# Kernel tuning notes

Hardware: AMD Instinct MI355X
Metric: run time of the kernel (lower is better)

Reference implementation:

```python
import jax, jax.numpy as jnp
import numpy as np

DELTA = 10.0
EPS = 1e-08
THRESHOLD = 0.9
STEEPNESS = 10.0


def setup_inputs() -> dict:
    key = jax.random.key(0)
    k1, k2 = jax.random.split(key)
    B, T2, T1, F = 16, 2048, 512, 128
    mels = jax.random.normal(k1, (B, T2, F), dtype=jnp.float32)
    alpha = jax.random.uniform(k2, (B, T2, T1), dtype=jnp.float32)
    mel_mask = jnp.ones((B, T2), dtype=jnp.int32)
    text_mask = jnp.ones((B, T1), dtype=jnp.int32)
    return {"mels": mels, "alpha": alpha, "mel_mask": mel_mask, "text_mask": text_mask}


def reference(mels, alpha, mel_mask, text_mask):
    B, T2, F = mels.shape
    T1 = text_mask.shape[-1]
    audio_mask = mel_mask.astype(bool)
    txt_mask = text_mask.astype(bool)
    am_f = audio_mask.astype(alpha.dtype)  # [B, T2]
    tm_f = txt_mask.astype(alpha.dtype)    # [B, T1]

    # index vector p: [B, T1]
    p = jnp.broadcast_to(jnp.arange(T1, dtype=alpha.dtype), (B, T1))

    # cosine similarity between consecutive frames (F.normalize: x / max(||x||, 1e-12))
    norm = jnp.maximum(jnp.linalg.norm(mels, axis=-1, keepdims=True), 1e-12)
    z_norm = mels / norm
    cosine_sim = jnp.sum(z_norm[:, :-1] * z_norm[:, 1:], axis=-1)  # [B, T2-1]
    activity = jax.nn.sigmoid(STEEPNESS * (THRESHOLD - cosine_sim))
    activity = jnp.concatenate([jnp.ones((B, 1), dtype=activity.dtype), activity], axis=-1)
    activity = activity * am_f

    # soft monotonic index via gated cumsum of alpha-proposal increments
    imv_proposal = jnp.einsum('bts,bs->bt', alpha, p)  # [B, T2]
    delta_prop = jnp.concatenate(
        [jnp.zeros((B, 1), dtype=imv_proposal.dtype), jnp.diff(imv_proposal, axis=-1)], axis=-1)
    eff_delta = jnp.clip(delta_prop * activity, 0.0, 1.0)
    imv = jnp.cumsum(eff_delta, axis=-1) * am_f

    # rescale so last valid frame maps to last phoneme index
    last_idx = jnp.maximum(audio_mask.sum(-1).astype(jnp.int32) - 1, 0)  # [B]
    last_val = jnp.maximum(jnp.take_along_axis(imv, last_idx[:, None], axis=1)[:, 0], 1e-06)
    text_len = txt_mask.sum(-1).astype(imv.dtype)
    scale = jnp.maximum(text_len - 1.0, 0.0) / last_val
    imv = imv * scale[:, None] * am_f

    # gamma: masked softmax over phonemes of -delta * (imv - p)^2
    dist_sq = (imv[:, :, None] - p[:, None, :]) ** 2  # [B, T2, T1]
    logits = jnp.where(txt_mask[:, None, :], -DELTA * dist_sq, -1e9)
    gamma = jax.nn.softmax(logits, axis=-1) * am_f[:, :, None]

    # durations: soft mass per phoneme
    durations = jnp.sum(gamma * am_f[:, :, None], axis=1) * tm_f  # [B, T1]

    # attention-pooling of mel frames onto phonemes
    w = jnp.swapaxes(gamma, 1, 2) * am_f[:, None, :]  # [B, T1, T2]
    w = w / (jnp.sum(w, axis=-1, keepdims=True) + EPS)
    aligned_mels = jnp.einsum('bst,btf->bsf', w, mels) * tm_f[:, :, None]  # [B, T1, F]
    return aligned_mels, durations, imv
```

## Files before the change

kernel.cpp:

```cpp
#include <hip/hip_runtime.h>
#include <math.h>
#include <cstddef>

#define B_  16
#define T2_ 2048
#define T1_ 512
#define F_  128

constexpr float DELTA_C  = 10.0f;
constexpr float EPS_C    = 1e-8f;
constexpr float THRESH_C = 0.9f;
constexpr float STEEP_C  = 10.0f;

typedef float f4v __attribute__((ext_vector_type(4)));

__global__ __launch_bounds__(256) void actprop_kernel(const float* __restrict__ mels,
                                                      const float* __restrict__ alpha,
                                                      const int* __restrict__ mel_mask,
                                                      float* __restrict__ act,
                                                      float* __restrict__ prop) {
    int wv   = (int)((blockIdx.x * blockDim.x + threadIdx.x) >> 6);
    int lane = threadIdx.x & 63;
    int il   = lane & 15;
    int r    = wv * 4 + (lane >> 4);
    int t    = r & (T2_ - 1);

    const f4v* arow = (const f4v*)(alpha + (size_t)r * T1_);
    f4v a0 = __builtin_nontemporal_load(&arow[il]);
    f4v a1 = __builtin_nontemporal_load(&arow[il + 16]);
    f4v a2 = __builtin_nontemporal_load(&arow[il + 32]);
    f4v a3 = __builtin_nontemporal_load(&arow[il + 48]);
    f4v a4 = __builtin_nontemporal_load(&arow[il + 64]);
    f4v a5 = __builtin_nontemporal_load(&arow[il + 80]);
    f4v a6 = __builtin_nontemporal_load(&arow[il + 96]);
    f4v a7 = __builtin_nontemporal_load(&arow[il + 112]);

    int rm = (t == 0) ? r : (r - 1);
    const f4v* my = (const f4v*)(mels + (size_t)r  * F_);
    const f4v* mx = (const f4v*)(mels + (size_t)rm * F_);
    f4v y0 = my[il * 2], y1 = my[il * 2 + 1];
    f4v x0 = mx[il * 2], x1 = mx[il * 2 + 1];

    float d  = x0.x*y0.x + x0.y*y0.y + x0.z*y0.z + x0.w*y0.w
             + x1.x*y1.x + x1.y*y1.y + x1.z*y1.z + x1.w*y1.w;
    float n0 = x0.x*x0.x + x0.y*x0.y + x0.z*x0.z + x0.w*x0.w
             + x1.x*x1.x + x1.y*x1.y + x1.z*x1.z + x1.w*x1.w;
    float n1 = y0.x*y0.x + y0.y*y0.y + y0.z*y0.z + y0.w*y0.w
             + y1.x*y1.x + y1.y*y1.y + y1.z*y1.z + y1.w*y1.w;

    float fb = (float)(il * 4);
    float psum;
    psum  = a0.x*(fb      ) + a0.y*(fb +   1.f) + a0.z*(fb +   2.f) + a0.w*(fb +   3.f);
    psum += a1.x*(fb+ 64.f) + a1.y*(fb +  65.f) + a1.z*(fb +  66.f) + a1.w*(fb +  67.f);
    psum += a2.x*(fb+128.f) + a2.y*(fb + 129.f) + a2.z*(fb + 130.f) + a2.w*(fb + 131.f);
    psum += a3.x*(fb+192.f) + a3.y*(fb + 193.f) + a3.z*(fb + 194.f) + a3.w*(fb + 195.f);
    psum += a4.x*(fb+256.f) + a4.y*(fb + 257.f) + a4.z*(fb + 258.f) + a4.w*(fb + 259.f);
    psum += a5.x*(fb+320.f) + a5.y*(fb + 321.f) + a5.z*(fb + 322.f) + a5.w*(fb + 323.f);
    psum += a6.x*(fb+384.f) + a6.y*(fb + 385.f) + a6.z*(fb + 386.f) + a6.w*(fb + 387.f);
    psum += a7.x*(fb+448.f) + a7.y*(fb + 449.f) + a7.z*(fb + 450.f) + a7.w*(fb + 451.f);

    for (int off = 8; off > 0; off >>= 1) {
        psum += __shfl_xor(psum, off, 64);
        d    += __shfl_xor(d,    off, 64);
        n0   += __shfl_xor(n0,   off, 64);
        n1   += __shfl_xor(n1,   off, 64);
    }

    if (il == 0) {
        float a_val;
        if (t == 0) {
            a_val = 1.0f;
        } else {
            float cs = d / (fmaxf(sqrtf(n0), 1e-12f) * fmaxf(sqrtf(n1), 1e-12f));
            a_val = 1.0f / (1.0f + __expf(-STEEP_C * (THRESH_C - cs)));
        }
        act[r]  = a_val * (float)mel_mask[r];
        prop[r] = psum;
    }
}

__global__ __launch_bounds__(512) void scan_kernel(const float* __restrict__ prop,
                                                   const float* __restrict__ act,
                                                   const int* __restrict__ mel_mask,
                                                   const int* __restrict__ text_mask,
                                                   float* __restrict__ imv_out,
                                                   float2* __restrict__ packed,
                                                   int2* __restrict__ bounds) {
    int b    = blockIdx.x;
    int tid  = threadIdx.x;
    int wave = tid >> 6, lane = tid & 63;
    __shared__ float s_imv[T2_];
    __shared__ float s_wsum[8];
    __shared__ int   s_am8[8], s_tm8[8];
    __shared__ int   s_tm[T1_];

    const float* pr = prop + (size_t)b * T2_;
    const float* ac = act  + (size_t)b * T2_;
    const int*   mm = mel_mask  + (size_t)b * T2_;
    const int*   tm = text_mask + (size_t)b * T1_;

    int tmv = tm[tid];
    s_tm[tid] = tmv;

    float e[4];
    int   mmv[4];
    int t0 = tid * 4;
    int am_local = 0;
    float run = 0.0f;
    for (int i = 0; i < 4; i++) {
        int t = t0 + i;
        float dd = (t == 0) ? 0.0f : (pr[t] - pr[t - 1]) * ac[t];
        dd = fminf(fmaxf(dd, 0.0f), 1.0f);
        run += dd;
        e[i] = run;
        mmv[i] = mm[t];
        am_local += mmv[i];
    }
    int tm_local = tmv;
    for (int off = 32; off > 0; off >>= 1) {
        am_local += __shfl_xor(am_local, off, 64);
        tm_local += __shfl_xor(tm_local, off, 64);
    }
    if (lane == 0) { s_am8[wave] = am_local; s_tm8[wave] = tm_local; }

    float v = run;
    for (int off = 1; off < 64; off <<= 1) {
        float u = __shfl_up(v, off, 64);
        if (lane >= off) v += u;
    }
    if (lane == 63) s_wsum[wave] = v;
    __syncthreads();

    float woff = 0.0f;
    for (int w = 0; w < 8; w++) woff += (w < wave) ? s_wsum[w] : 0.0f;
    float excl = woff + v - run;
    for (int i = 0; i < 4; i++) {
        int t = t0 + i;
        s_imv[t] = (e[i] + excl) * (float)mmv[i];
    }
    __syncthreads();

    int am_total = 0, tm_total = 0;
    for (int w = 0; w < 8; w++) { am_total += s_am8[w]; tm_total += s_tm8[w]; }
    int last_idx = max(am_total - 1, 0);
    float last_val = fmaxf(s_imv[last_idx], 1e-6f);
    float scale = fmaxf((float)tm_total - 1.0f, 0.0f) / last_val;
    __syncthreads();

    for (int i = 0; i < 4; i++) {
        int t = t0 + i;
        int valid = mmv[i];
        float vv = s_imv[t] * scale * (float)valid;
        imv_out[(size_t)b * T2_ + t] = vv;
        int c = (int)floorf(vv);
        float Z = 0.0f;
        for (int s = c - 2; s <= c + 3; s++) {
            if (s >= 0 && s < T1_ && s_tm[s]) {
                float dd = vv - (float)s;
                Z += __expf(-DELTA_C * dd * dd);
            }
        }
        Z = fmaxf(Z, 1e-30f);
        float key = valid ? vv : 3.0e4f;
        float2 pk = {key, valid ? (1.0f / Z) : 0.0f};
        packed[(size_t)b * T2_ + t] = pk;
        s_imv[t] = key;
    }
    __syncthreads();

    {
        int s = tid;
        float lov = (float)s - 3.0f, hiv = (float)s + 3.0f;
        int lo = 0, hi = T2_;
        while (lo < hi) { int mid = (lo + hi) >> 1; if (s_imv[mid] >= lov) hi = mid; else lo = mid + 1; }
        int st = lo;
        hi = T2_;
        while (lo < hi) { int mid = (lo + hi) >> 1; if (s_imv[mid] > hiv) hi = mid; else lo = mid + 1; }
        int2 be = {st, lo};
        bounds[(size_t)b * T1_ + s] = be;
    }
}

__global__ __launch_bounds__(256) void pool_kernel(const float* __restrict__ mels,
                                                   const int* __restrict__ text_mask,
                                                   const float2* __restrict__ packed,
                                                   const int2* __restrict__ bounds,
                                                   float* __restrict__ aligned,
                                                   float* __restrict__ dur) {
    int wid  = (int)((blockIdx.x * blockDim.x + threadIdx.x) >> 6);
    int lane = threadIdx.x & 63;
    if (wid >= B_ * (T1_ / 2)) return;
    int b = wid >> 8, s0 = (wid & 255) * 2;
    int half = lane >> 5, hl = lane & 31;
    float fs0 = (float)s0, fs1 = fs0 + 1.0f;

    const float2* pk   = packed + (size_t)b * T2_;
    const f4v*    mel4 = (const f4v*)(mels + (size_t)b * T2_ * F_);
    int2 b0 = bounds[(size_t)b * T1_ + s0];
    int2 b1 = bounds[(size_t)b * T1_ + s0 + 1];
    int t_lo = b0.x, t_hi = b1.y;

    float ax0 = 0.f, ay0 = 0.f, az0 = 0.f, aw0 = 0.f, g0s = 0.f;
    float ax1 = 0.f, ay1 = 0.f, az1 = 0.f, aw1 = 0.f, g1s = 0.f;
    for (int t = t_lo; t < t_hi; t += 2) {
        int  tl = t + half;
        bool on = tl < t_hi;
        int  ts = on ? tl : t;
        float2 p = pk[ts];
        f4v    m = mel4[(size_t)ts * 32 + hl];
        float d0 = p.x - fs0, d1 = p.x - fs1;
        float g0 = on ? __expf(-DELTA_C * d0 * d0) * p.y : 0.0f;
        float g1 = on ? __expf(-DELTA_C * d1 * d1) * p.y : 0.0f;
        g0s += g0; g1s += g1;
        ax0 += g0 * m.x; ay0 += g0 * m.y; az0 += g0 * m.z; aw0 += g0 * m.w;
        ax1 += g1 * m.x; ay1 += g1 * m.y; az1 += g1 * m.z; aw1 += g1 * m.w;
    }

    g0s += __shfl_xor(g0s, 32, 64);
    g1s += __shfl_xor(g1s, 32, 64);
    ax0 += __shfl_xor(ax0, 32, 64);
    ay0 += __shfl_xor(ay0, 32, 64);
    az0 += __shfl_xor(az0, 32, 64);
    aw0 += __shfl_xor(aw0, 32, 64);
    ax1 += __shfl_xor(ax1, 32, 64);
    ay1 += __shfl_xor(ay1, 32, 64);
    az1 += __shfl_xor(az1, 32, 64);
    aw1 += __shfl_xor(aw1, 32, 64);

    float tm0 = (float)text_mask[(size_t)b * T1_ + s0];
    float tm1 = (float)text_mask[(size_t)b * T1_ + s0 + 1];
    float inv0 = tm0 / (g0s + EPS_C);
    float inv1 = tm1 / (g1s + EPS_C);

    f4v out;
    if (half == 0) {
        out.x = ax0 * inv0; out.y = ay0 * inv0; out.z = az0 * inv0; out.w = aw0 * inv0;
    } else {
        out.x = ax1 * inv1; out.y = ay1 * inv1; out.z = az1 * inv1; out.w = aw1 * inv1;
    }
    float* obase = aligned + ((size_t)b * T1_ + s0 + half) * F_;
    ((f4v*)obase)[hl] = out;
    if (lane == 0)  dur[(size_t)b * T1_ + s0]     = g0s * tm0;
    if (lane == 32) dur[(size_t)b * T1_ + s0 + 1] = g1s * tm1;
}

extern "C" void kernel_launch(void* const* d_in, const int* in_sizes, int n_in,
                              void* d_out, int out_size, void* d_ws, size_t ws_size,
                              hipStream_t stream) {
    const float* mels      = (const float*)d_in[0];
    const float* alpha     = (const float*)d_in[1];
    const int*   mel_mask  = (const int*)d_in[2];
    const int*   text_mask = (const int*)d_in[3];

    float* out     = (float*)d_out;
    float* aligned = out;
    float* dur     = out + (size_t)B_ * T1_ * F_;
    float* imv     = dur + (size_t)B_ * T1_;

    float*  ws     = (float*)d_ws;
    float*  act    = ws;
    float*  prop   = ws + (size_t)B_ * T2_;
    float2* packed = (float2*)(ws + 2 * (size_t)B_ * T2_);
    int2*   bounds = (int2*)(ws + 4 * (size_t)B_ * T2_);

    actprop_kernel<<<(B_ * T2_) / 16, dim3(256), 0, stream>>>(mels, alpha, mel_mask, act, prop);
    scan_kernel   <<<B_,              dim3(512), 0, stream>>>(prop, act, mel_mask, text_mask, imv, packed, bounds);
    pool_kernel   <<<(B_ * T1_ / 2) / 4, dim3(256), 0, stream>>>(mels, text_mask, packed, bounds, aligned, dur);
}
```

Before: 128.4 us.

## Fuse activity, scan and pooling kernels into one flag-synchronized kernel

Merges the three kernels into one launch of 1024 blocks. Each block first computes activity and proposal values for 32 frames, then bumps a per-batch counter. One block per batch spins until all 64 blocks of that batch are done, runs the scan and bounds search with 256 threads (8 elements per thread), and releases a per-batch flag. The other blocks wait on that flag and then do the pooling. The aim is to drop the inter-kernel launch gaps and let batches proceed independently instead of stalling at global kernel boundaries. In exchange it needs every block resident at once to avoid deadlock, halves the scan's thread count, and adds a memset for the flags.

```diff
diff --git a/kernel.cpp b/kernel.cpp
--- a/kernel.cpp
+++ b/kernel.cpp
@@ -14,234 +14,258 @@
 
 typedef float f4v __attribute__((ext_vector_type(4)));
 
-__global__ __launch_bounds__(256) void actprop_kernel(const float* __restrict__ mels,
-                                                      const float* __restrict__ alpha,
-                                                      const int* __restrict__ mel_mask,
-                                                      float* __restrict__ act,
-                                                      float* __restrict__ prop) {
-    int wv   = (int)((blockIdx.x * blockDim.x + threadIdx.x) >> 6);
-    int lane = threadIdx.x & 63;
-    int il   = lane & 15;
-    int r    = wv * 4 + (lane >> 4);
-    int t    = r & (T2_ - 1);
-
-    const f4v* arow = (const f4v*)(alpha + (size_t)r * T1_);
-    f4v a0 = __builtin_nontemporal_load(&arow[il]);
-    f4v a1 = __builtin_nontemporal_load(&arow[il + 16]);
-    f4v a2 = __builtin_nontemporal_load(&arow[il + 32]);
-    f4v a3 = __builtin_nontemporal_load(&arow[il + 48]);
-    f4v a4 = __builtin_nontemporal_load(&arow[il + 64]);
-    f4v a5 = __builtin_nontemporal_load(&arow[il + 80]);
-    f4v a6 = __builtin_nontemporal_load(&arow[il + 96]);
-    f4v a7 = __builtin_nontemporal_load(&arow[il + 112]);
-
-    int rm = (t == 0) ? r : (r - 1);
-    const f4v* my = (const f4v*)(mels + (size_t)r  * F_);
-    const f4v* mx = (const f4v*)(mels + (size_t)rm * F_);
-    f4v y0 = my[il * 2], y1 = my[il * 2 + 1];
-    f4v x0 = mx[il * 2], x1 = mx[il * 2 + 1];
-
-    float d  = x0.x*y0.x + x0.y*y0.y + x0.z*y0.z + x0.w*y0.w
-             + x1.x*y1.x + x1.y*y1.y + x1.z*y1.z + x1.w*y1.w;
-    float n0 = x0.x*x0.x + x0.y*x0.y + x0.z*x0.z + x0.w*x0.w
-             + x1.x*x1.x + x1.y*x1.y + x1.z*x1.z + x1.w*x1.w;
-    float n1 = y0.x*y0.x + y0.y*y0.y + y0.z*y0.z + y0.w*y0.w
-             + y1.x*y1.x + y1.y*y1.y + y1.z*y1.z + y1.w*y1.w;
-
-    float fb = (float)(il * 4);
-    float psum;
-    psum  = a0.x*(fb      ) + a0.y*(fb +   1.f) + a0.z*(fb +   2.f) + a0.w*(fb +   3.f);
-    psum += a1.x*(fb+ 64.f) + a1.y*(fb +  65.f) + a1.z*(fb +  66.f) + a1.w*(fb +  67.f);
-    psum += a2.x*(fb+128.f) + a2.y*(fb + 129.f) + a2.z*(fb + 130.f) + a2.w*(fb + 131.f);
-    psum += a3.x*(fb+192.f) + a3.y*(fb + 193.f) + a3.z*(fb + 194.f) + a3.w*(fb + 195.f);
-    psum += a4.x*(fb+256.f) + a4.y*(fb + 257.f) + a4.z*(fb + 258.f) + a4.w*(fb + 259.f);
-    psum += a5.x*(fb+320.f) + a5.y*(fb + 321.f) + a5.z*(fb + 322.f) + a5.w*(fb + 323.f);
-    psum += a6.x*(fb+384.f) + a6.y*(fb + 385.f) + a6.z*(fb + 386.f) + a6.w*(fb + 387.f);
-    psum += a7.x*(fb+448.f) + a7.y*(fb + 449.f) + a7.z*(fb + 450.f) + a7.w*(fb + 451.f);
-
-    for (int off = 8; off > 0; off >>= 1) {
-        psum += __shfl_xor(psum, off, 64);
-        d    += __shfl_xor(d,    off, 64);
-        n0   += __shfl_xor(n0,   off, 64);
-        n1   += __shfl_xor(n1,   off, 64);
-    }
-
-    if (il == 0) {
-        float a_val;
-        if (t == 0) {
-            a_val = 1.0f;
-        } else {
-            float cs = d / (fmaxf(sqrtf(n0), 1e-12f) * fmaxf(sqrtf(n1), 1e-12f));
-            a_val = 1.0f / (1.0f + __expf(-STEEP_C * (THRESH_C - cs)));
-        }
-        act[r]  = a_val * (float)mel_mask[r];
-        prop[r] = psum;
-    }
-}
-
-__global__ __launch_bounds__(512) void scan_kernel(const float* __restrict__ prop,
-                                                   const float* __restrict__ act,
-                                                   const int* __restrict__ mel_mask,
-                                                   const int* __restrict__ text_mask,
-                                                   float* __restrict__ imv_out,
-                                                   float2* __restrict__ packed,
-                                                   int2* __restrict__ bounds) {
-    int b    = blockIdx.x;
-    int tid  = threadIdx.x;
-    int wave = tid >> 6, lane = tid & 63;
+__global__ __launch_bounds__(256, 4) void fused_kernel(
+        const float* __restrict__ mels,
+        const float* __restrict__ alpha,
+        const int* __restrict__ mel_mask,
+        const int* __restrict__ text_mask,
+        float* __restrict__ act,
+        float* __restrict__ prop,
+        float* __restrict__ imv_out,
+        float2* __restrict__ packed,
+        int2* __restrict__ bounds,
+        float* __restrict__ aligned,
+        float* __restrict__ dur,
+        int* done_act,
+        int* scan_done)
+{
     __shared__ float s_imv[T2_];
-    __shared__ float s_wsum[8];
-    __shared__ int   s_am8[8], s_tm8[8];
+    __shared__ float s_wsum[4];
+    __shared__ int   s_am4[4], s_tm4[4];
     __shared__ int   s_tm[T1_];
 
-    const float* pr = prop + (size_t)b * T2_;
-    const float* ac = act  + (size_t)b * T2_;
-    const int*   mm = mel_mask  + (size_t)b * T2_;
-    const int*   tm = text_mask + (size_t)b * T1_;
-
-    int tmv = tm[tid];
-    s_tm[tid] = tmv;
-
-    float e[4];
-    int   mmv[4];
-    int t0 = tid * 4;
-    int am_local = 0;
-    float run = 0.0f;
-    for (int i = 0; i < 4; i++) {
-        int t = t0 + i;
-        float dd = (t == 0) ? 0.0f : (pr[t] - pr[t - 1]) * ac[t];
-        dd = fminf(fmaxf(dd, 0.0f), 1.0f);
-        run += dd;
-        e[i] = run;
-        mmv[i] = mm[t];
-        am_local += mmv[i];
-    }
-    int tm_local = tmv;
-    for (int off = 32; off > 0; off >>= 1) {
-        am_local += __shfl_xor(am_local, off, 64);
-        tm_local += __shfl_xor(tm_local, off, 64);
-    }
-    if (lane == 0) { s_am8[wave] = am_local; s_tm8[wave] = tm_local; }
-
-    float v = run;
-    for (int off = 1; off < 64; off <<= 1) {
-        float u = __shfl_up(v, off, 64);
-        if (lane >= off) v += u;
-    }
-    if (lane == 63) s_wsum[wave] = v;
-    __syncthreads();
-
-    float woff = 0.0f;
-    for (int w = 0; w < 8; w++) woff += (w < wave) ? s_wsum[w] : 0.0f;
-    float excl = woff + v - run;
-    for (int i = 0; i < 4; i++) {
-        int t = t0 + i;
-        s_imv[t] = (e[i] + excl) * (float)mmv[i];
+    const int g    = blockIdx.x;
+    const int b    = g >> 6;
+    const int tid  = threadIdx.x;
+    const int wv   = tid >> 6, lane = tid & 63;
+    const int il   = lane & 15, sub = lane >> 4;
+
+    #pragma unroll
+    for (int p = 0; p < 2; ++p) {
+        int r = g * 32 + p * 16 + wv * 4 + sub;
+        int t = r & (T2_ - 1);
+
+        const f4v* arow = (const f4v*)(alpha + (size_t)r * T1_);
+        f4v a0 = __builtin_nontemporal_load(&arow[il]);
+        f4v a1 = __builtin_nontemporal_load(&arow[il + 16]);
+        f4v a2 = __builtin_nontemporal_load(&arow[il + 32]);
+        f4v a3 = __builtin_nontemporal_load(&arow[il + 48]);
+        f4v a4 = __builtin_nontemporal_load(&arow[il + 64]);
+        f4v a5 = __builtin_nontemporal_load(&arow[il + 80]);
+        f4v a6 = __builtin_nontemporal_load(&arow[il + 96]);
+        f4v a7 = __builtin_nontemporal_load(&arow[il + 112]);
+
+        int rm = (t == 0) ? r : (r - 1);
+        const f4v* my = (const f4v*)(mels + (size_t)r  * F_);
+        const f4v* mx = (const f4v*)(mels + (size_t)rm * F_);
+        f4v y0 = my[il * 2], y1 = my[il * 2 + 1];
+        f4v x0 = mx[il * 2], x1 = mx[il * 2 + 1];
+
+        float d  = x0.x*y0.x + x0.y*y0.y + x0.z*y0.z + x0.w*y0.w
+                 + x1.x*y1.x + x1.y*y1.y + x1.z*y1.z + x1.w*y1.w;
+        float n0 = x0.x*x0.x + x0.y*x0.y + x0.z*x0.z + x0.w*x0.w
+                 + x1.x*x1.x + x1.y*x1.y + x1.z*x1.z + x1.w*x1.w;
+        float n1 = y0.x*y0.x + y0.y*y0.y + y0.z*y0.z + y0.w*y0.w
+                 + y1.x*y1.x + y1.y*y1.y + y1.z*y1.z + y1.w*y1.w;
+
+        float fb = (float)(il * 4);
+        float psum;
+        psum  = a0.x*(fb      ) + a0.y*(fb +   1.f) + a0.z*(fb +   2.f) + a0.w*(fb +   3.f);
+        psum += a1.x*(fb+ 64.f) + a1.y*(fb +  65.f) + a1.z*(fb +  66.f) + a1.w*(fb +  67.f);
+        psum += a2.x*(fb+128.f) + a2.y*(fb + 129.f) + a2.z*(fb + 130.f) + a2.w*(fb + 131.f);
+        psum += a3.x*(fb+192.f) + a3.y*(fb + 193.f) + a3.z*(fb + 194.f) + a3.w*(fb + 195.f);
+        psum += a4.x*(fb+256.f) + a4.y*(fb + 257.f) + a4.z*(fb + 258.f) + a4.w*(fb + 259.f);
+        psum += a5.x*(fb+320.f) + a5.y*(fb + 321.f) + a5.z*(fb + 322.f) + a5.w*(fb + 323.f);
+        psum += a6.x*(fb+384.f) + a6.y*(fb + 385.f) + a6.z*(fb + 386.f) + a6.w*(fb + 387.f);
+        psum += a7.x*(fb+448.f) + a7.y*(fb + 449.f) + a7.z*(fb + 450.f) + a7.w*(fb + 451.f);
+
+        for (int off = 8; off > 0; off >>= 1) {
+            psum += __shfl_xor(psum, off, 64);
+            d    += __shfl_xor(d,    off, 64);
+            n0   += __shfl_xor(n0,   off, 64);
+            n1   += __shfl_xor(n1,   off, 64);
+        }
+
+        if (il == 0) {
+            float a_val;
+            if (t == 0) {
+                a_val = 1.0f;
+            } else {
+                float cs = d / (fmaxf(sqrtf(n0), 1e-12f) * fmaxf(sqrtf(n1), 1e-12f));
+                a_val = 1.0f / (1.0f + __expf(-STEEP_C * (THRESH_C - cs)));
+            }
+            act[r]  = a_val * (float)mel_mask[r];
+            prop[r] = psum;
+        }
     }
     __syncthreads();
-
-    int am_total = 0, tm_total = 0;
-    for (int w = 0; w < 8; w++) { am_total += s_am8[w]; tm_total += s_tm8[w]; }
-    int last_idx = max(am_total - 1, 0);
-    float last_val = fmaxf(s_imv[last_idx], 1e-6f);
-    float scale = fmaxf((float)tm_total - 1.0f, 0.0f) / last_val;
-    __syncthreads();
-
-    for (int i = 0; i < 4; i++) {
-        int t = t0 + i;
-        int valid = mmv[i];
-        float vv = s_imv[t] * scale * (float)valid;
-        imv_out[(size_t)b * T2_ + t] = vv;
-        int c = (int)floorf(vv);
-        float Z = 0.0f;
-        for (int s = c - 2; s <= c + 3; s++) {
-            if (s >= 0 && s < T1_ && s_tm[s]) {
-                float dd = vv - (float)s;
-                Z += __expf(-DELTA_C * dd * dd);
+    if (tid == 0)
+        __hip_atomic_fetch_add(&done_act[b], 1, __ATOMIC_RELEASE, __HIP_MEMORY_SCOPE_AGENT);
+
+    const bool is_scan = ((g & 63) == 0);
+
+    if (is_scan) {
+        const int* tm = text_mask + (size_t)b * T1_;
+        int tmv0 = tm[tid], tmv1 = tm[tid + 256];
+        s_tm[tid] = tmv0; s_tm[tid + 256] = tmv1;
+
+        if (lane == 0) {
+            while (__hip_atomic_load(&done_act[b], __ATOMIC_RELAXED, __HIP_MEMORY_SCOPE_AGENT) < 64)
+                __builtin_amdgcn_s_sleep(2);
+        }
+        __builtin_amdgcn_fence(__ATOMIC_ACQUIRE, "agent");
+        __syncthreads();
+
+        const float* pr_ = prop + (size_t)b * T2_;
+        const float* ac_ = act  + (size_t)b * T2_;
+        const int*   mm_ = mel_mask + (size_t)b * T2_;
+
+        float e[8];
+        int   mmv[8];
+        int t0 = tid * 8;
+        int am_local = 0;
+        float run = 0.0f;
+        #pragma unroll
+        for (int i = 0; i < 8; i++) {
+            int t = t0 + i;
+            float dd = (t == 0) ? 0.0f : (pr_[t] - pr_[t - 1]) * ac_[t];
+            dd = fminf(fmaxf(dd, 0.0f), 1.0f);
+            run += dd;
+            e[i] = run;
+            mmv[i] = mm_[t];
+            am_local += mmv[i];
+        }
+        int tm_local = tmv0 + tmv1;
+        for (int off = 32; off > 0; off >>= 1) {
+            am_local += __shfl_xor(am_local, off, 64);
+            tm_local += __shfl_xor(tm_local, off, 64);
+        }
+        if (lane == 0) { s_am4[wv] = am_local; s_tm4[wv] = tm_local; }
+
+        float v = run;
+        for (int off = 1; off < 64; off <<= 1) {
+            float u = __shfl_up(v, off, 64);
+            if (lane >= off) v += u;
+        }
+        if (lane == 63) s_wsum[wv] = v;
+        __syncthreads();
+
+        float woff = 0.0f;
+        for (int w = 0; w < 4; w++) woff += (w < wv) ? s_wsum[w] : 0.0f;
+        float excl = woff + v - run;
+        #pragma unroll
+        for (int i = 0; i < 8; i++) {
+            int t = t0 + i;
+            s_imv[t] = (e[i] + excl) * (float)mmv[i];
+        }
+        __syncthreads();
+
+        int am_total = s_am4[0] + s_am4[1] + s_am4[2] + s_am4[3];
+        int tm_total = s_tm4[0] + s_tm4[1] + s_tm4[2] + s_tm4[3];
+        int last_idx = max(am_total - 1, 0);
+        float last_val = fmaxf(s_imv[last_idx], 1e-6f);
+        float scale = fmaxf((float)tm_total - 1.0f, 0.0f) / last_val;
+        __syncthreads();
+
+        #pragma unroll
+        for (int i = 0; i < 8; i++) {
+            int t = t0 + i;
+            int valid = mmv[i];
+            float vv = s_imv[t] * scale * (float)valid;
+            imv_out[(size_t)b * T2_ + t] = vv;
+            int c = (int)floorf(vv);
+            float Z = 0.0f;
+            for (int s = c - 2; s <= c + 3; s++) {
+                if (s >= 0 && s < T1_ && s_tm[s]) {
+                    float dd = vv - (float)s;
+                    Z += __expf(-DELTA_C * dd * dd);
+                }
             }
-        }
-        Z = fmaxf(Z, 1e-30f);
-        float key = valid ? vv : 3.0e4f;
-        float2 pk = {key, valid ? (1.0f / Z) : 0.0f};
-        packed[(size_t)b * T2_ + t] = pk;
-        s_imv[t] = key;
+            Z = fmaxf(Z, 1e-30f);
+            float key = valid ? vv : 3.0e4f;
+            float2 pkv = {key, valid ? (1.0f / Z) : 0.0f};
+            packed[(size_t)b * T2_ + t] = pkv;
+            s_imv[t] = key;
+        }
+        __syncthreads();
+
+        for (int k = 0; k < 2; k++) {
+            int s = tid + k * 256;
+            float lov = (float)s - 3.0f, hiv = (float)s + 3.0f;
+            int lo = 0, hi = T2_;
+            while (lo < hi) { int mid = (lo + hi) >> 1; if (s_imv[mid] >= lov) hi = mid; else lo = mid + 1; }
+            int st = lo;
+            hi = T2_;
+            while (lo < hi) { int mid = (lo + hi) >> 1; if (s_imv[mid] > hiv) hi = mid; else lo = mid + 1; }
+            int2 be = {st, lo};
+            bounds[(size_t)b * T1_ + s] = be;
+        }
+        __syncthreads();
+        if (tid == 0)
+            __hip_atomic_store(&scan_done[b], 1, __ATOMIC_RELEASE, __HIP_MEMORY_SCOPE_AGENT);
+    } else {
+        if (lane == 0) {
+            while (__hip_atomic_load(&scan_done[b], __ATOMIC_RELAXED, __HIP_MEMORY_SCOPE_AGENT) == 0)
+                __builtin_amdgcn_s_sleep(2);
+        }
+        __builtin_amdgcn_fence(__ATOMIC_ACQUIRE, "agent");
     }
-    __syncthreads();
 
     {
-        int s = tid;
-        float lov = (float)s - 3.0f, hiv = (float)s + 3.0f;
-        int lo = 0, hi = T2_;
-        while (lo < hi) { int mid = (lo + hi) >> 1; if (s_imv[mid] >= lov) hi = mid; else lo = mid + 1; }
-        int st = lo;
-        hi = T2_;
-        while (lo < hi) { int mid = (lo + hi) >> 1; if (s_imv[mid] > hiv) hi = mid; else lo = mid + 1; }
-        int2 be = {st, lo};
-        bounds[(size_t)b * T1_ + s] = be;
+        int pairi = (g & 63) * 4 + wv;
+        int s0 = pairi * 2;
+        int half = lane >> 5, hl = lane & 31;
+        float fs0 = (float)s0, fs1 = fs0 + 1.0f;
+
+        const float2* pk   = packed + (size_t)b * T2_;
+        const f4v*    mel4 = (const f4v*)(mels + (size_t)b * T2_ * F_);
+        int2 b0 = bounds[(size_t)b * T1_ + s0];
+        int2 b1 = bounds[(size_t)b * T1_ + s0 + 1];
+        int t_lo = b0.x, t_hi = b1.y;
+
+        float ax0 = 0.f, ay0 = 0.f, az0 = 0.f, aw0 = 0.f, g0s = 0.f;
+        float ax1 = 0.f, ay1 = 0.f, az1 = 0.f, aw1 = 0.f, g1s = 0.f;
+        for (int t = t_lo; t < t_hi; t += 2) {
+            int  tl = t + half;
+            bool on = tl < t_hi;
+            int  ts = on ? tl : t;
+            float2 p = pk[ts];
+            f4v    m = mel4[(size_t)ts * 32 + hl];
+            float d0 = p.x - fs0, d1 = p.x - fs1;
+            float g0 = on ? __expf(-DELTA_C * d0 * d0) * p.y : 0.0f;
+            float g1 = on ? __expf(-DELTA_C * d1 * d1) * p.y : 0.0f;
+            g0s += g0; g1s += g1;
+            ax0 += g0 * m.x; ay0 += g0 * m.y; az0 += g0 * m.z; aw0 += g0 * m.w;
+            ax1 += g1 * m.x; ay1 += g1 * m.y; az1 += g1 * m.z; aw1 += g1 * m.w;
+        }
+
+        g0s += __shfl_xor(g0s, 32, 64);
+        g1s += __shfl_xor(g1s, 32, 64);
+        ax0 += __shfl_xor(ax0, 32, 64);
+        ay0 += __shfl_xor(ay0, 32, 64);
+        az0 += __shfl_xor(az0, 32, 64);
+        aw0 += __shfl_xor(aw0, 32, 64);
+        ax1 += __shfl_xor(ax1, 32, 64);
+        ay1 += __shfl_xor(ay1, 32, 64);
+        az1 += __shfl_xor(az1, 32, 64);
+        aw1 += __shfl_xor(aw1, 32, 64);
+
+        float tm0 = (float)text_mask[(size_t)b * T1_ + s0];
+        float tm1 = (float)text_mask[(size_t)b * T1_ + s0 + 1];
+        float inv0 = tm0 / (g0s + EPS_C);
+        float inv1 = tm1 / (g1s + EPS_C);
+
+        f4v outv;
+        if (half == 0) {
+            outv.x = ax0 * inv0; outv.y = ay0 * inv0; outv.z = az0 * inv0; outv.w = aw0 * inv0;
+        } else {
+            outv.x = ax1 * inv1; outv.y = ay1 * inv1; outv.z = az1 * inv1; outv.w = aw1 * inv1;
+        }
+        float* obase = aligned + ((size_t)b * T1_ + s0 + half) * F_;
+        ((f4v*)obase)[hl] = outv;
+        if (lane == 0)  dur[(size_t)b * T1_ + s0]     = g0s * tm0;
+        if (lane == 32) dur[(size_t)b * T1_ + s0 + 1] = g1s * tm1;
     }
-}
-
-__global__ __launch_bounds__(256) void pool_kernel(const float* __restrict__ mels,
-                                                   const int* __restrict__ text_mask,
-                                                   const float2* __restrict__ packed,
-                                                   const int2* __restrict__ bounds,
-                                                   float* __restrict__ aligned,
-                                                   float* __restrict__ dur) {
-    int wid  = (int)((blockIdx.x * blockDim.x + threadIdx.x) >> 6);
-    int lane = threadIdx.x & 63;
-    if (wid >= B_ * (T1_ / 2)) return;
-    int b = wid >> 8, s0 = (wid & 255) * 2;
-    int half = lane >> 5, hl = lane & 31;
-    float fs0 = (float)s0, fs1 = fs0 + 1.0f;
-
-    const float2* pk   = packed + (size_t)b * T2_;
-    const f4v*    mel4 = (const f4v*)(mels + (size_t)b * T2_ * F_);
-    int2 b0 = bounds[(size_t)b * T1_ + s0];
-    int2 b1 = bounds[(size_t)b * T1_ + s0 + 1];
-    int t_lo = b0.x, t_hi = b1.y;
-
-    float ax0 = 0.f, ay0 = 0.f, az0 = 0.f, aw0 = 0.f, g0s = 0.f;
-    float ax1 = 0.f, ay1 = 0.f, az1 = 0.f, aw1 = 0.f, g1s = 0.f;
-    for (int t = t_lo; t < t_hi; t += 2) {
-        int  tl = t + half;
-        bool on = tl < t_hi;
-        int  ts = on ? tl : t;
-        float2 p = pk[ts];
-        f4v    m = mel4[(size_t)ts * 32 + hl];
-        float d0 = p.x - fs0, d1 = p.x - fs1;
-        float g0 = on ? __expf(-DELTA_C * d0 * d0) * p.y : 0.0f;
-        float g1 = on ? __expf(-DELTA_C * d1 * d1) * p.y : 0.0f;
-        g0s += g0; g1s += g1;
-        ax0 += g0 * m.x; ay0 += g0 * m.y; az0 += g0 * m.z; aw0 += g0 * m.w;
-        ax1 += g1 * m.x; ay1 += g1 * m.y; az1 += g1 * m.z; aw1 += g1 * m.w;
-    }
-
-    g0s += __shfl_xor(g0s, 32, 64);
-    g1s += __shfl_xor(g1s, 32, 64);
-    ax0 += __shfl_xor(ax0, 32, 64);
-    ay0 += __shfl_xor(ay0, 32, 64);
-    az0 += __shfl_xor(az0, 32, 64);
-    aw0 += __shfl_xor(aw0, 32, 64);
-    ax1 += __shfl_xor(ax1, 32, 64);
-    ay1 += __shfl_xor(ay1, 32, 64);
-    az1 += __shfl_xor(az1, 32, 64);
-    aw1 += __shfl_xor(aw1, 32, 64);
-
-    float tm0 = (float)text_mask[(size_t)b * T1_ + s0];
-    float tm1 = (float)text_mask[(size_t)b * T1_ + s0 + 1];
-    float inv0 = tm0 / (g0s + EPS_C);
-    float inv1 = tm1 / (g1s + EPS_C);
-
-    f4v out;
-    if (half == 0) {
-        out.x = ax0 * inv0; out.y = ay0 * inv0; out.z = az0 * inv0; out.w = aw0 * inv0;
-    } else {
-        out.x = ax1 * inv1; out.y = ay1 * inv1; out.z = az1 * inv1; out.w = aw1 * inv1;
-    }
-    float* obase = aligned + ((size_t)b * T1_ + s0 + half) * F_;
-    ((f4v*)obase)[hl] = out;
-    if (lane == 0)  dur[(size_t)b * T1_ + s0]     = g0s * tm0;
-    if (lane == 32) dur[(size_t)b * T1_ + s0 + 1] = g1s * tm1;
 }
 
 extern "C" void kernel_launch(void* const* d_in, const int* in_sizes, int n_in,
@@ -262,8 +286,11 @@
     float*  prop   = ws + (size_t)B_ * T2_;
     float2* packed = (float2*)(ws + 2 * (size_t)B_ * T2_);
     int2*   bounds = (int2*)(ws + 4 * (size_t)B_ * T2_);
-
-    actprop_kernel<<<(B_ * T2_) / 16, dim3(256), 0, stream>>>(mels, alpha, mel_mask, act, prop);
-    scan_kernel   <<<B_,              dim3(512), 0, stream>>>(prop, act, mel_mask, text_mask, imv, packed, bounds);
-    pool_kernel   <<<(B_ * T1_ / 2) / 4, dim3(256), 0, stream>>>(mels, text_mask, packed, bounds, aligned, dur);
+    int*    flags  = (int*)((char*)d_ws + (1 << 20));
+
+    hipMemsetAsync(flags, 0, 32 * sizeof(int), stream);
+
+    fused_kernel<<<1024, dim3(256), 0, stream>>>(mels, alpha, mel_mask, text_mask,
+                                                 act, prop, imv, packed, bounds,
+                                                 aligned, dur, flags, flags + 16);
 }
```

Result: slower. 279.3 us (+117.6%).
